# Kernel tuning notes

Hardware: AMD Instinct MI355X
Metric: run time of the kernel (lower is better)

Reference implementation:

```python
import jax, jax.numpy as jnp
import numpy as np

B, N, DIM, H, DH = 1, 2048, 1024, 16, 64


def setup_inputs() -> dict:
    key = jax.random.key(0)
    k1, k2, k3 = jax.random.split(key, 3)
    x = jax.random.normal(k1, (B, N, DIM), dtype=jnp.float32)
    # LinearNoBias(dim, 6*heads*dim_head): weight [6*H*DH, DIM]
    w_qkv = jax.random.normal(k2, (6 * H * DH, DIM), dtype=jnp.float32) * (DIM ** -0.5)
    # LinearNoBias(heads*dim_head, dim): weight [DIM, H*DH]
    w_out = jax.random.normal(k3, (DIM, H * DH), dtype=jnp.float32) * ((H * DH) ** -0.5)
    return {"x": x, "w_qkv": w_qkv, "w_out": w_out}


def reference(x, w_qkv, w_out):
    b, n, _ = x.shape
    scale = DH ** -0.5
    qkvs = x @ w_qkv.T  # [b, n, 6*H*DH]
    # rearrange 'b n (qkv h d) -> qkv b h n d'
    qkvs = qkvs.reshape(b, n, 6, H, DH).transpose(2, 0, 3, 1, 4)
    qu, ku, vu, qc, kc, vc = qkvs
    qu = qu * scale
    qc = qc * scale

    upper = jnp.triu(jnp.ones((n, n), dtype=bool), 1)  # strict upper triangle

    # term1: causal (lower-incl-diag) qc . vu
    term1 = jnp.einsum('bhid,bhjd->bhij', qc, vu)
    term1 = jnp.where(upper, 0.0, term1)

    # sigmoid lookahead term: strict-upper only
    sig = jax.nn.sigmoid(jnp.einsum('bhid,bhjd->bhij', qu, ku))
    sig = jnp.where(upper, sig, 0.0)

    Su = jnp.einsum('bhij,bhkj->bhik', term1, sig)

    Sc = jnp.einsum('bhid,bhjd->bhij', qc, kc)
    neg = -jnp.finfo(Sc.dtype).max
    Sc = jnp.where(upper, neg, Sc)

    scores = Sc - jax.nn.silu(Su)
    attn = jax.nn.softmax(scores, axis=-1)
    out = jnp.einsum('bhij,bhjd->bhid', attn, vc)  # [b,h,n,d]
    out = out.transpose(0, 2, 1, 3).reshape(b, n, H * DH)
    return out @ w_out.T
```

## Files before the change

### kernel.cpp

```cpp
#include <hip/hip_runtime.h>

using f16 = _Float16;
using half8  = __attribute__((ext_vector_type(8))) f16;
using half4v = __attribute__((ext_vector_type(4))) f16;
using float4v = __attribute__((ext_vector_type(4))) float;

#define DEV static __device__ __forceinline__

constexpr int N = 2048, DIM = 1024, H = 16, DH = 64, F6 = 6144;
constexpr int LDSH = 136;
constexpr int TS = 128 * 128;
constexpr int NTILES = 136;
constexpr int KD = 2048 * 64;


DEV int PL(int i, int k) { return i * (i + 1) / 2 + k; }
DEV int PU(int a, int b) { return a * 16 - a * (a - 1) / 2 + (b - a); }

template<int ROWS, int THREADS>
DEV void stage64(const f16* __restrict__ g, int strideHalves, f16* lds, int tid) {
#pragma unroll
  for (int q = 0; q < (ROWS * 8) / THREADS; ++q) {
    const int chunk = q * THREADS + tid;
    const int m = chunk >> 3, c = (chunk & 7) ^ (m & 7);
    const f16* gp = g + (size_t)m * strideHalves + c * 8;
    __builtin_amdgcn_global_load_lds(
        (const __attribute__((address_space(1))) unsigned int*)gp,
        (__attribute__((address_space(3))) unsigned int*)(lds + chunk * 8), 16, 0, 0);
  }
}

template<int ELEMS, int THREADS>
DEV void stage_panel(const f16* __restrict__ g, f16* lds, int tid) {
#pragma unroll
  for (int i = 0; i < ELEMS / 8 / THREADS; ++i) {
    const int chunk = i * THREADS + tid;
    __builtin_amdgcn_global_load_lds(
        (const __attribute__((address_space(1))) unsigned int*)(g + (size_t)chunk * 8),
        (__attribute__((address_space(3))) unsigned int*)(lds + chunk * 8), 16, 0, 0);
  }
}

DEV half8 rdfrag(const f16* T, int m, int ks, int q) {
  const int c = (ks * 4 + q) ^ (m & 7);
  return *(const half8*)(T + m * 64 + c * 8);
}

DEV void wfrag(f16* T, int row, int col, f16 v) {
  T[row * 64 + ((((col >> 3) ^ (row & 7)) << 3) | (col & 7))] = v;
}

DEV void gemm64(const f16* As, const f16* Bs, int wm, int wn, int l, float4v acc[4][4]) {
  const int q = l >> 4, mm = l & 15;
#pragma unroll
  for (int ks = 0; ks < 2; ++ks) {
    half8 af[4], bf[4];
#pragma unroll
    for (int mi = 0; mi < 4; ++mi) af[mi] = rdfrag(As, wm + mm + mi * 16, ks, q);
#pragma unroll
    for (int ni = 0; ni < 4; ++ni) bf[ni] = rdfrag(Bs, wn + mm + ni * 16, ks, q);
#pragma unroll
    for (int mi = 0; mi < 4; ++mi)
#pragma unroll
      for (int ni = 0; ni < 4; ++ni)
        acc[mi][ni] = __builtin_amdgcn_mfma_f32_16x16x32_f16(af[mi], bf[ni], acc[mi][ni], 0, 0, 0);
  }
}

DEV void decode_pair(int p, int& ti, int& tk) {
  int t = (int)((sqrtf(8.f * p + 1.f) - 1.f) * 0.5f);
  while (t * (t + 1) / 2 > p) --t;
  while ((t + 1) * (t + 2) / 2 <= p) ++t;
  const int i2 = p - t * (t + 1) / 2;
  ti = (15 - t) + i2;
  tk = i2;
}

__global__ __launch_bounds__(256) void k_cast(const float* __restrict__ s, f16* __restrict__ d, int n4) {
  int i = blockIdx.x * 256 + threadIdx.x;
  if (i < n4) {
    float4 v = ((const float4*)s)[i];
    half4v h;
    h[0] = (f16)v.x; h[1] = (f16)v.y; h[2] = (f16)v.z; h[3] = (f16)v.w;
    ((half4v*)d)[i] = h;
  }
}

__global__ __launch_bounds__(256) void k_qkv(const f16* __restrict__ xh, const f16* __restrict__ wh,
                                             f16* __restrict__ quh, f16* __restrict__ kuh,
                                             f16* __restrict__ vuh, f16* __restrict__ qch,
                                             f16* __restrict__ kch, f16* __restrict__ vcT,
                                             f16* __restrict__ vuT) {
  __shared__ __align__(16) f16 lds[128 * LDSH];
  f16* As = lds; f16* Bs = lds + 128 * 64;
  const int tid = threadIdx.x, w = tid >> 6, l = tid & 63;
  const int tm = blockIdx.x * 128, tf = blockIdx.y * 128;
  const int wm = (w >> 1) * 64, wn = (w & 1) * 64;
  float4v acc[4][4] = {};
  for (int k0 = 0; k0 < DIM; k0 += 64) {
    stage64<128, 256>(xh + (size_t)tm * DIM + k0, DIM, As, tid);
    stage64<128, 256>(wh + (size_t)tf * DIM + k0, DIM, Bs, tid);
    __syncthreads();
    gemm64(As, Bs, wm, wn, l, acc);
    __syncthreads();
  }
  const int rbase = (l >> 4) * 4, cidx = l & 15;
  const int t = tf >> 10;
  const float sc = (t == 0 || t == 3) ? 0.125f : 1.f;
  if (t == 5 || t == 2) {
#pragma unroll
    for (int mi = 0; mi < 4; ++mi)
#pragma unroll
      for (int ni = 0; ni < 4; ++ni) {
        const int f = tf + wn + ni * 16 + cidx;
        const int h = (f & 1023) >> 6, d = f & 63;
        const int n = tm + wm + mi * 16 + rbase;
        half4v p;
#pragma unroll
        for (int r = 0; r < 4; ++r) p[r] = (f16)acc[mi][ni][r];
        if (t == 5) {
          const int ks2 = (n & 63) >> 5, q2 = (n >> 3) & 3;
          const int inner = ks2 * 256 + q2 * 64 + (d >> 4) * 16 + (d & 15);
          *(half4v*)(vcT + (size_t)h * DH * N + (size_t)(n >> 6) * 4096 +
                     (size_t)inner * 8 + (n & 7)) = p;
        } else {
          *(half4v*)(vuT + ((size_t)h * DH + d) * N + n) = p;
        }
      }
  }
  if (t != 5) {
#pragma unroll
    for (int mi = 0; mi < 4; ++mi)
#pragma unroll
      for (int ni = 0; ni < 4; ++ni)
#pragma unroll
        for (int r = 0; r < 4; ++r)
          lds[(wm + mi * 16 + rbase + r) * LDSH + wn + ni * 16 + cidx] = (f16)(acc[mi][ni][r] * sc);
    __syncthreads();
    const int hb = (tf & 1023) >> 6;
    if (t == 4) {
#pragma unroll
      for (int qq = 0; qq < 8; ++qq) {
        const int idx = qq * 256 + tid;
        const int hh = idx >> 10, f = idx & 1023;
        const int pl = f >> 9, inner = f & 511;
        const int m2 = inner & 15, ni2 = (inner >> 4) & 3, q2 = (inner >> 6) & 3, ks2 = inner >> 8;
        const int row = pl * 64 + ni2 * 16 + m2;
        const int col = hh * 64 + ks2 * 32 + q2 * 8;
        *(half8*)(kch + (size_t)(hb + hh) * N * DH + ((size_t)(tm >> 6) + pl) * 4096 +
                  (size_t)inner * 8) = *(const half8*)(lds + row * LDSH + col);
      }
    } else {
      f16* dst = (t == 0) ? quh : (t == 1) ? kuh : (t == 2) ? vuh : qch;
#pragma unroll
      for (int q = 0; q < 8; ++q) {
        const int idx = q * 256 + tid, row = idx >> 4, c = idx & 15;
        const int h = hb + (c >> 3), d0 = (c & 7) * 8, n = tm + row;
        *(half8*)(dst + ((size_t)h * N + n) * DH + d0) = *(const half8*)(lds + row * LDSH + c * 8);
      }
    }
  }
}

__global__ __launch_bounds__(256) void k_dsig(const f16* __restrict__ quh, const f16* __restrict__ kuh,
                                              const f16* __restrict__ qch, const f16* __restrict__ vuh,
                                              const f16* __restrict__ vuT,
                                              f16* __restrict__ sigb, f16* __restrict__ DC,
                                              f16* __restrict__ diagb, int h0) {
  __shared__ __align__(16) f16 L[32768];
  f16* quA = L; f16* kuB = L + 8192; f16* s1 = L + 16384; f16* s2 = L + 24576;
  int b, a;
  decode_pair(blockIdx.y, b, a);
  const int hl = blockIdx.x, h = h0 + hl;
  const int tid = threadIdx.x, w = tid >> 6, l = tid & 63;
  const int q = l >> 4, m = l & 15;
  const int wm = (w >> 1) * 64, wn = (w & 1) * 64;
  const size_t ho = (size_t)h * N * DH;

  stage64<128, 256>(quh + ho + (size_t)(a * 128) * DH, DH, quA, tid);
  stage64<128, 256>(kuh + ho + (size_t)(b * 128) * DH, DH, kuB, tid);
  __syncthreads();
  float4v acc[4][4] = {};
  gemm64(quA, kuB, wm, wn, l, acc);
  __syncthreads();
  stage64<64, 256>(vuT + (size_t)h * DH * N + b * 128, N, kuB, tid);
  stage64<64, 256>(vuT + (size_t)h * DH * N + b * 128 + 64, N, kuB + 4096, tid);
#pragma unroll
  for (int mi = 0; mi < 4; ++mi)
#pragma unroll
    for (int ni = 0; ni < 4; ++ni)
#pragma unroll
      for (int r = 0; r < 4; ++r) {
        const int row = wm + mi * 16 + q * 4 + r;
        const int col = wn + ni * 16 + m;
        const float x = acc[mi][ni][r];
        const f16 sv = (b * 128 + col > a * 128 + row)
                           ? (f16)__builtin_amdgcn_rcpf(1.f + __expf(-x)) : (f16)0.f;
        wfrag((col < 64) ? s1 : s2, row, col & 63, sv);
      }
  __syncthreads();
  {
    f16* Sg = sigb + ((size_t)hl * NTILES + PU(a, b)) * TS;
#pragma unroll
    for (int qq = 0; qq < 8; ++qq) {
      const int idx = qq * 256 + tid;
      const int hf = idx >> 10, inner = idx & 1023;
      const int m2 = inner & 15, ni2 = (inner >> 4) & 3, q2 = (inner >> 6) & 3, ks2 = inner >> 8;
      const int row = hf * 64 + ni2 * 16 + m2;
      const int c8 = ks2 * 4 + q2;
      const f16* p = ((c8 >> 3) ? s2 : s1) + row * 64 + (((c8 & 7) ^ (row & 7)) << 3);
      *(half8*)(Sg + (size_t)idx * 8) = *(const half8*)p;
    }
  }
  float4v dacc[2][4] = {};
#pragma unroll
  for (int p = 0; p < 2; ++p)
#pragma unroll
    for (int ks = 0; ks < 2; ++ks) {
      half8 bf[4], af[2];
#pragma unroll
      for (int ni = 0; ni < 4; ++ni) bf[ni] = rdfrag(kuB + p * 4096, ni * 16 + m, ks, q);
#pragma unroll
      for (int mi = 0; mi < 2; ++mi) af[mi] = rdfrag(p ? s2 : s1, w * 32 + mi * 16 + m, ks, q);
#pragma unroll
      for (int mi = 0; mi < 2; ++mi)
#pragma unroll
        for (int ni = 0; ni < 4; ++ni)
          dacc[mi][ni] = __builtin_amdgcn_mfma_f32_16x16x32_f16(af[mi], bf[ni], dacc[mi][ni], 0, 0, 0);
    }
  __syncthreads();
  if (a == b) {
    stage64<128, 256>(qch + ho + (size_t)(a * 128) * DH, DH, quA, tid);
    stage64<128, 256>(vuh + ho + (size_t)(a * 128) * DH, DH, kuB, tid);
  }
  {
    f16* epsD = s1;
#pragma unroll
    for (int mi = 0; mi < 2; ++mi)
#pragma unroll
      for (int ni = 0; ni < 4; ++ni)
#pragma unroll
        for (int r = 0; r < 4; ++r)
          epsD[(w * 32 + mi * 16 + q * 4 + r) * 68 + ni * 16 + m] = (f16)dacc[mi][ni][r];
    __syncthreads();
    f16* Dg = DC + ((size_t)hl * 16 + b) * KD + (size_t)a * 8192;
#pragma unroll
    for (int qq = 0; qq < 4; ++qq) {
      const int idx = qq * 256 + tid;
      const int pl = idx >> 9, inner = idx & 511;
      const int m2 = inner & 15, ni2 = (inner >> 4) & 3, q2 = (inner >> 6) & 3, ks2 = inner >> 8;
      const int row = pl * 64 + ni2 * 16 + m2;
      const int c = ks2 * 4 + q2;
      *(half8*)(Dg + (size_t)idx * 8) = *(const half8*)(epsD + row * 68 + c * 8);
    }
  }
  if (a == b) {
    float4v tacc[4][4] = {};
    gemm64(quA, kuB, wm, wn, l, tacc);
    f16* Tg = diagb + ((size_t)hl * 16 + a) * TS;
#pragma unroll
    for (int mi = 0; mi < 4; ++mi)
#pragma unroll
      for (int ni = 0; ni < 4; ++ni)
#pragma unroll
        for (int r = 0; r < 4; ++r) {
          const int row = wm + mi * 16 + q * 4 + r, col = wn + ni * 16 + m;
          Tg[(size_t)row * 128 + col] = (col <= row) ? (f16)tacc[mi][ni][r] : (f16)0.f;
        }
  }
}

__global__ __launch_bounds__(256) void k_scan(f16* __restrict__ DC, int total) {
  const int idx = blockIdx.x * 256 + threadIdx.x;
  if (idx >= total) return;
  const int g = idx >> 17, off = idx & (KD - 1);
  const int a = off >> 13;
  f16* p = DC + (size_t)g * 16 * KD + off;
  float s = 0.f;
#pragma unroll
  for (int T = 0; T < 16; ++T) {
    const float v = (T >= a) ? (float)p[(size_t)T * KD] : 0.f;
    p[(size_t)T * KD] = (f16)s;
    s += v;
  }
}

__global__ __launch_bounds__(256) void k_favs(const f16* __restrict__ qch, const f16* __restrict__ kch,
                                              const f16* __restrict__ DC, const f16* __restrict__ sigb,
                                              const f16* __restrict__ diagb, const f16* __restrict__ vcT,
                                              f16* __restrict__ Oh, int h0) {
  __shared__ __align__(16) f16 L[2 * 16384 + 4 * 1024];
  const int hl = blockIdx.x, h = h0 + hl;
  const int y = (int)blockIdx.y;
  const int mt = (y < 32) ? (63 - y) : (y - 32);
  const int tid = threadIdx.x, w = tid >> 6, l = tid & 63;
  const int q = l >> 4, m = l & 15;
  const int d = w >> 1;
  const int rw = w & 1;
  const int ti = mt >> 2, r0 = mt * 32;
  const size_t ho = (size_t)h * N * DH;
  const f16* qc = qch + ho;
  const f16* kcb = kch + ho;
  const f16* Cb = DC + ((size_t)hl * 16 + ti) * KD;
  const f16* Td = diagb + ((size_t)hl * 16 + ti) * TS;
  const f16* Sgb = sigb + (size_t)hl * NTILES * TS;
  const f16* V = vcT + (size_t)h * DH * N;
  f16* pw = L + 32768 + w * 1024;
  const int lo = q * 512 + m * 8;
  constexpr float L2E = 1.44269504f;
  constexpr float THR2 = 11.5416f;

  const int rr = rw * 16 + m;
  half8 qcA[2], tdA[4];
  const int dr = (mt & 3) * 32 + rr;
#pragma unroll
  for (int ks = 0; ks < 2; ++ks)
    qcA[ks] = *(const half8*)(qc + (size_t)(r0 + rr) * DH + ks * 32 + q * 8);
#pragma unroll
  for (int ks = 0; ks < 4; ++ks)
    tdA[ks] = *(const half8*)(Td + (size_t)dr * 128 + ks * 32 + q * 8);

  float4v o[4] = {};
  float mrun[4], lrun[4];
#pragma unroll
  for (int r = 0; r < 4; ++r) { mrun[r] = -1e30f; lrun[r] = 0.f; }

  const int jtmax = mt >> 1;
  const int np = jtmax / 2 + 1;
  stage_panel<16384, 256>(Sgb + (size_t)PU(0, ti) * TS, L, tid);
  half8 cC[2][4];
  {
    int c0 = d; if (c0 > jtmax) c0 = 0;
    const f16* Cp = Cb + (size_t)c0 * 4096 + lo;
#pragma unroll
    for (int ks = 0; ks < 2; ++ks)
#pragma unroll
      for (int ni = 0; ni < 4; ++ni) cC[ks][ni] = *(const half8*)(Cp + ks * 2048 + ni * 128);
  }

  for (int p = 0; p < np; ++p) {
    const int pn = (p + 1 <= ti) ? (p + 1) : ti;
    stage_panel<16384, 256>(Sgb + (size_t)PU(pn, ti) * TS,
                            L + ((p + 1) & 1) * 16384, tid);
    half8 nC[2][4];
    {
      int c2 = 2 * (p + 1) + d; if (c2 > jtmax) c2 = 0;
      const f16* Cp = Cb + (size_t)c2 * 4096 + lo;
#pragma unroll
      for (int ks = 0; ks < 2; ++ks)
#pragma unroll
        for (int ni = 0; ni < 4; ++ni) nC[ks][ni] = *(const half8*)(Cp + ks * 2048 + ni * 128);
    }
    asm volatile("s_waitcnt vmcnt(16)" ::: "memory");
    __builtin_amdgcn_s_barrier();
    __builtin_amdgcn_sched_barrier(0);

    const int c = 2 * p + d;
    if (c <= jtmax) {
      const f16* Sp = L + (p & 1) * 16384 + d * 8192 + lo;
      const f16* Kp = kcb + (size_t)c * 4096 + lo;
      const f16* Vp = V + (size_t)c * 4096 + lo;
      half8 bK[2][4];
#pragma unroll
      for (int ks = 0; ks < 2; ++ks)
#pragma unroll
        for (int ni = 0; ni < 4; ++ni) bK[ks][ni] = *(const half8*)(Kp + ks * 2048 + ni * 128);
      float4v s[4] = {};
#pragma unroll
      for (int ks = 0; ks < 2; ++ks)
#pragma unroll
        for (int ni = 0; ni < 4; ++ni)
          s[ni] = __builtin_amdgcn_mfma_f32_16x16x32_f16(qcA[ks], cC[ks][ni], s[ni], 0, 0, 0);
#pragma unroll
      for (int ks = 0; ks < 4; ++ks) {
        half8 bf[4];
#pragma unroll
        for (int ni = 0; ni < 4; ++ni) bf[ni] = *(const half8*)(Sp + ks * 2048 + ni * 128);
#pragma unroll
        for (int ni = 0; ni < 4; ++ni)
          s[ni] = __builtin_amdgcn_mfma_f32_16x16x32_f16(tdA[ks], bf[ni], s[ni], 0, 0, 0);
      }
      half8 bV[2][4];
#pragma unroll
      for (int ks = 0; ks < 2; ++ks)
#pragma unroll
        for (int ni = 0; ni < 4; ++ni) bV[ks][ni] = *(const half8*)(Vp + ks * 2048 + ni * 128);
#pragma unroll
      for (int ni = 0; ni < 4; ++ni)
#pragma unroll
        for (int r = 0; r < 4; ++r) {
          const float x = s[ni][r];
          s[ni][r] = -x * __builtin_amdgcn_rcpf(1.f + __expf(-x));
        }
#pragma unroll
      for (int ks = 0; ks < 2; ++ks)
#pragma unroll
        for (int ni = 0; ni < 4; ++ni)
          s[ni] = __builtin_amdgcn_mfma_f32_16x16x32_f16(qcA[ks], bK[ks][ni], s[ni], 0, 0, 0);
      if (c == jtmax) {
        const int k0 = c * 64;
#pragma unroll
        for (int ni = 0; ni < 4; ++ni) {
          const int col = k0 + ni * 16 + m;
#pragma unroll
          for (int r = 0; r < 4; ++r) {
            const int gr = r0 + rw * 16 + q * 4 + r;
            if (col > gr) s[ni][r] = -1e30f;
          }
        }
      }
#pragma unroll
      for (int ni = 0; ni < 4; ++ni)
#pragma unroll
        for (int r = 0; r < 4; ++r) s[ni][r] *= L2E;
      float ts[4];
#pragma unroll
      for (int r = 0; r < 4; ++r) {
        float tmx = fmaxf(fmaxf(s[0][r], s[1][r]), fmaxf(s[2][r], s[3][r]));
#pragma unroll
        for (int x = 1; x < 16; x <<= 1) tmx = fmaxf(tmx, __shfl_xor(tmx, x));
        if (tmx > mrun[r] + THR2) {
          const float al = __builtin_amdgcn_exp2f(mrun[r] - tmx);
          mrun[r] = tmx;
          lrun[r] *= al;
#pragma unroll
          for (int ni = 0; ni < 4; ++ni) o[ni][r] *= al;
        }
        ts[r] = 0.f;
      }
#pragma unroll
      for (int ni = 0; ni < 4; ++ni)
#pragma unroll
        for (int r = 0; r < 4; ++r) {
          const float pp = __builtin_amdgcn_exp2f(s[ni][r] - mrun[r]);
          wfrag(pw, q * 4 + r, ni * 16 + m, (f16)pp);
          ts[r] += pp;
        }
#pragma unroll
      for (int r = 0; r < 4; ++r) {
#pragma unroll
        for (int x = 1; x < 16; x <<= 1) ts[r] += __shfl_xor(ts[r], x);
        lrun[r] += ts[r];
      }
#pragma unroll
      for (int ks = 0; ks < 2; ++ks) {
        half8 af = rdfrag(pw, m, ks, q);
#pragma unroll
        for (int ni = 0; ni < 4; ++ni)
          o[ni] = __builtin_amdgcn_mfma_f32_16x16x32_f16(af, bV[ks][ni], o[ni], 0, 0, 0);
      }
    }
    __builtin_amdgcn_sched_barrier(0);
    __builtin_amdgcn_s_barrier();
#pragma unroll
    for (int ks = 0; ks < 2; ++ks)
#pragma unroll
      for (int ni = 0; ni < 4; ++ni) cC[ks][ni] = nC[ks][ni];
  }

  asm volatile("s_waitcnt vmcnt(0)" ::: "memory");
  __builtin_amdgcn_s_barrier();

  float* OB = (float*)L;
  float* MB = (float*)L + 2 * 16 * 68;
  float* LB = MB + 2 * 16;
  if (d == 1) {
#pragma unroll
    for (int ni = 0; ni < 4; ++ni)
#pragma unroll
      for (int r = 0; r < 4; ++r)
        OB[(rw * 16 + q * 4 + r) * 68 + ni * 16 + m] = o[ni][r];
    if (m == 0)
#pragma unroll
      for (int r = 0; r < 4; ++r) {
        MB[rw * 16 + q * 4 + r] = mrun[r];
        LB[rw * 16 + q * 4 + r] = lrun[r];
      }
  }
  __syncthreads();
  if (d == 0) {
#pragma unroll
    for (int r = 0; r < 4; ++r) {
      const int row = q * 4 + r;
      const float m2 = MB[rw * 16 + row], l2 = LB[rw * 16 + row];
      const float ms = fmaxf(mrun[r], m2);
      const float e1 = __builtin_amdgcn_exp2f(mrun[r] - ms);
      const float e2 = __builtin_amdgcn_exp2f(m2 - ms);
      const float inv = __builtin_amdgcn_rcpf(lrun[r] * e1 + l2 * e2);
      const int gr = r0 + rw * 16 + row;
#pragma unroll
      for (int ni = 0; ni < 4; ++ni) {
        const float ov = o[ni][r] * e1 + OB[(rw * 16 + row) * 68 + ni * 16 + m] * e2;
        Oh[(size_t)gr * (H * DH) + h * DH + ni * 16 + m] = (f16)(ov * inv);
      }
    }
  }
}

__global__ __launch_bounds__(256) void k_out(const f16* __restrict__ Oh, const f16* __restrict__ wo,
                                             float* __restrict__ out) {
  __shared__ __align__(16) f16 lds[128 * LDSH];
  f16* As = lds; f16* Bs = lds + 128 * 64;
  const int tid = threadIdx.x, w = tid >> 6, l = tid & 63;
  const int tm = blockIdx.x * 128, tn = blockIdx.y * 128;
  const int wm = (w >> 1) * 64, wn = (w & 1) * 64;
  float4v acc[4][4] = {};
  for (int k0 = 0; k0 < DIM; k0 += 64) {
    stage64<128, 256>(Oh + (size_t)tm * DIM + k0, DIM, As, tid);
    stage64<128, 256>(wo + (size_t)tn * DIM + k0, DIM, Bs, tid);
    __syncthreads();
    gemm64(As, Bs, wm, wn, l, acc);
    __syncthreads();
  }
  const int rbase = (l >> 4) * 4, cidx = l & 15;
#pragma unroll
  for (int mi = 0; mi < 4; ++mi)
#pragma unroll
    for (int ni = 0; ni < 4; ++ni)
#pragma unroll
      for (int r = 0; r < 4; ++r) {
        const int n = tm + wm + mi * 16 + rbase + r;
        const int dmo = tn + wn + ni * 16 + cidx;
        out[(size_t)n * DIM + dmo] = acc[mi][ni][r];
      }
}

extern "C" void kernel_launch(void* const* d_in, const int* in_sizes, int n_in,
                              void* d_out, int out_size, void* d_ws, size_t ws_size,
                              hipStream_t stream) {
  const float* x = (const float*)d_in[0];
  const float* wqkv = (const float*)d_in[1];
  const float* wout = (const float*)d_in[2];
  float* out = (float*)d_out;
  char* ws = (char*)d_ws;

  size_t off = 0;
  auto alloc = [&](size_t b) { size_t o = off; off += (b + 255) & ~(size_t)255; return o; };
  f16* xh  = (f16*)(ws + alloc((size_t)N * DIM * 2));
  f16* wqh = (f16*)(ws + alloc((size_t)F6 * DIM * 2));
  f16* woh = (f16*)(ws + alloc((size_t)DIM * H * DH * 2));
  f16* quh = (f16*)(ws + alloc((size_t)H * N * DH * 2));
  f16* kuh = (f16*)(ws + alloc((size_t)H * N * DH * 2));
  f16* vuh = (f16*)(ws + alloc((size_t)H * N * DH * 2));
  f16* qch = (f16*)(ws + alloc((size_t)H * N * DH * 2));
  f16* kch = (f16*)(ws + alloc((size_t)H * N * DH * 2));
  f16* vcT = (f16*)(ws + alloc((size_t)H * DH * N * 2));
  f16* vuT = (f16*)(ws + alloc((size_t)H * DH * N * 2));
  f16* Oh  = (f16*)(ws + alloc((size_t)N * H * DH * 2));
  const size_t persist = off;

  const size_t per_head = ((size_t)NTILES * TS + (size_t)16 * KD + (size_t)16 * TS) * 2;
  int G = (ws_size > persist + 4096) ? (int)((ws_size - persist - 4096) / per_head) : 1;
  if (G < 1) G = 1;
  if (G > 16) G = 16;
  {
    const int R = (H + G - 1) / G;
    G = (H + R - 1) / R;
  }
  f16* sigb  = (f16*)(ws + alloc((size_t)G * NTILES * TS * 2));
  f16* DC    = (f16*)(ws + alloc((size_t)G * 16 * KD * 2));
  f16* diagb = (f16*)(ws + alloc((size_t)G * 16 * TS * 2));

  k_cast<<<(N * DIM / 4 + 255) / 256, 256, 0, stream>>>(x, xh, N * DIM / 4);
  k_cast<<<(F6 * DIM / 4 + 255) / 256, 256, 0, stream>>>(wqkv, wqh, F6 * DIM / 4);
  k_cast<<<(DIM * H * DH / 4 + 255) / 256, 256, 0, stream>>>(wout, woh, DIM * H * DH / 4);

  k_qkv<<<dim3(N / 128, F6 / 128), 256, 0, stream>>>(xh, wqh, quh, kuh, vuh, qch, kch, vcT, vuT);

  for (int h0 = 0; h0 < H; h0 += G) {
    const int Gr = (H - h0 < G) ? (H - h0) : G;
    k_dsig<<<dim3(Gr, 136), 256, 0, stream>>>(quh, kuh, qch, vuh, vuT, sigb, DC, diagb, h0);
    k_scan<<<(Gr * KD + 255) / 256, 256, 0, stream>>>(DC, Gr * KD);
    k_favs<<<dim3(Gr, 64), 256, 0, stream>>>(qch, kch, DC, sigb, diagb, vcT, Oh, h0);
  }

  k_out<<<dim3(16, 8), 256, 0, stream>>>(Oh, woh, out);
}
```

Measured before the change: 283.0 us.

## Split favs key range across two blocks per row tile and merge partials

Each row tile of the attention kernel is now handled by two blocks that each process half of the key panels. Each block writes unnormalized fp32 partial outputs plus running max and sum, and a new merge kernel combines them into fp16 Oh. This doubles the grid to improve occupancy and load balance on the causal triangle. The cost is extra global traffic for the partials, one more launch, and the lazy rescale threshold being replaced by an unconditional rescale.

New measurement: 280.9 us. No clear change (-0.7%).

```diff
diff --git a/kernel.cpp b/kernel.cpp
--- a/kernel.cpp
+++ b/kernel.cpp
@@ -288,11 +288,13 @@
 __global__ __launch_bounds__(256) void k_favs(const f16* __restrict__ qch, const f16* __restrict__ kch,
                                               const f16* __restrict__ DC, const f16* __restrict__ sigb,
                                               const f16* __restrict__ diagb, const f16* __restrict__ vcT,
-                                              f16* __restrict__ Oh, int h0) {
+                                              float* __restrict__ Opart, float* __restrict__ mpart,
+                                              float* __restrict__ lpart, int h0) {
   __shared__ __align__(16) f16 L[2 * 16384 + 4 * 1024];
   const int hl = blockIdx.x, h = h0 + hl;
   const int y = (int)blockIdx.y;
-  const int mt = (y < 32) ? (63 - y) : (y - 32);
+  const int mt = 63 - (y >> 1);
+  const int hf = y & 1;
   const int tid = threadIdx.x, w = tid >> 6, l = tid & 63;
   const int q = l >> 4, m = l & 15;
   const int d = w >> 1;
@@ -308,7 +310,6 @@
   f16* pw = L + 32768 + w * 1024;
   const int lo = q * 512 + m * 8;
   constexpr float L2E = 1.44269504f;
-  constexpr float THR2 = 11.5416f;
 
   const int rr = rw * 16 + m;
   half8 qcA[2], tdA[4];
@@ -327,10 +328,14 @@
 
   const int jtmax = mt >> 1;
   const int np = jtmax / 2 + 1;
-  stage_panel<16384, 256>(Sgb + (size_t)PU(0, ti) * TS, L, tid);
+  const int p0 = hf ? (np + 1) / 2 : 0;
+  const int p1 = hf ? np : (np + 1) / 2;
+
+  const int ps0 = (p0 <= ti) ? p0 : ti;
+  stage_panel<16384, 256>(Sgb + (size_t)PU(ps0, ti) * TS, L + (p0 & 1) * 16384, tid);
   half8 cC[2][4];
   {
-    int c0 = d; if (c0 > jtmax) c0 = 0;
+    int c0 = 2 * p0 + d; if (c0 > jtmax) c0 = 0;
     const f16* Cp = Cb + (size_t)c0 * 4096 + lo;
 #pragma unroll
     for (int ks = 0; ks < 2; ++ks)
@@ -338,7 +343,7 @@
       for (int ni = 0; ni < 4; ++ni) cC[ks][ni] = *(const half8*)(Cp + ks * 2048 + ni * 128);
   }
 
-  for (int p = 0; p < np; ++p) {
+  for (int p = p0; p < p1; ++p) {
     const int pn = (p + 1 <= ti) ? (p + 1) : ti;
     stage_panel<16384, 256>(Sgb + (size_t)PU(pn, ti) * TS,
                             L + ((p + 1) & 1) * 16384, tid);
@@ -419,13 +424,12 @@
         float tmx = fmaxf(fmaxf(s[0][r], s[1][r]), fmaxf(s[2][r], s[3][r]));
 #pragma unroll
         for (int x = 1; x < 16; x <<= 1) tmx = fmaxf(tmx, __shfl_xor(tmx, x));
-        if (tmx > mrun[r] + THR2) {
-          const float al = __builtin_amdgcn_exp2f(mrun[r] - tmx);
-          mrun[r] = tmx;
-          lrun[r] *= al;
-#pragma unroll
-          for (int ni = 0; ni < 4; ++ni) o[ni][r] *= al;
-        }
+        const float nm = fmaxf(mrun[r], tmx);
+        const float al = __builtin_amdgcn_exp2f(mrun[r] - nm);
+        mrun[r] = nm;
+        lrun[r] *= al;
+#pragma unroll
+        for (int ni = 0; ni < 4; ++ni) o[ni][r] *= al;
         ts[r] = 0.f;
       }
 #pragma unroll
@@ -479,6 +483,9 @@
   }
   __syncthreads();
   if (d == 0) {
+    float* Op = Opart + (size_t)(hl * 2 + hf) * N * 64;
+    float* Mp = mpart + (hl * 2 + hf) * N;
+    float* Lp = lpart + (hl * 2 + hf) * N;
 #pragma unroll
     for (int r = 0; r < 4; ++r) {
       const int row = q * 4 + r;
@@ -486,14 +493,41 @@
       const float ms = fmaxf(mrun[r], m2);
       const float e1 = __builtin_amdgcn_exp2f(mrun[r] - ms);
       const float e2 = __builtin_amdgcn_exp2f(m2 - ms);
-      const float inv = __builtin_amdgcn_rcpf(lrun[r] * e1 + l2 * e2);
       const int gr = r0 + rw * 16 + row;
-#pragma unroll
-      for (int ni = 0; ni < 4; ++ni) {
-        const float ov = o[ni][r] * e1 + OB[(rw * 16 + row) * 68 + ni * 16 + m] * e2;
-        Oh[(size_t)gr * (H * DH) + h * DH + ni * 16 + m] = (f16)(ov * inv);
-      }
+      if (m == 0) { Mp[gr] = ms; Lp[gr] = lrun[r] * e1 + l2 * e2; }
+#pragma unroll
+      for (int ni = 0; ni < 4; ++ni)
+        Op[(size_t)gr * 64 + ni * 16 + m] =
+            o[ni][r] * e1 + OB[(rw * 16 + row) * 68 + ni * 16 + m] * e2;
     }
+  }
+}
+
+__global__ __launch_bounds__(256) void k_merge(const float* __restrict__ Opart,
+                                               const float* __restrict__ mpart,
+                                               const float* __restrict__ lpart,
+                                               f16* __restrict__ Oh, int h0) {
+  const int hl = blockIdx.x, h = h0 + hl;
+  const float* O0 = Opart + (size_t)(hl * 2 + 0) * N * 64;
+  const float* O1 = Opart + (size_t)(hl * 2 + 1) * N * 64;
+#pragma unroll
+  for (int it = 0; it < 2; ++it) {
+    const int idx = (int)blockIdx.y * 512 + it * 256 + threadIdx.x;
+    const int row = idx >> 4, c4 = idx & 15;
+    const float m0 = mpart[(hl * 2 + 0) * N + row], m1 = mpart[(hl * 2 + 1) * N + row];
+    const float l0 = lpart[(hl * 2 + 0) * N + row], l1 = lpart[(hl * 2 + 1) * N + row];
+    const float ms = fmaxf(m0, m1);
+    const float e0 = __builtin_amdgcn_exp2f(m0 - ms);
+    const float e1 = __builtin_amdgcn_exp2f(m1 - ms);
+    const float inv = __builtin_amdgcn_rcpf(l0 * e0 + l1 * e1);
+    const float4 a = ((const float4*)(O0 + (size_t)row * 64))[c4];
+    const float4 b = ((const float4*)(O1 + (size_t)row * 64))[c4];
+    half4v o4;
+    o4[0] = (f16)((a.x * e0 + b.x * e1) * inv);
+    o4[1] = (f16)((a.y * e0 + b.y * e1) * inv);
+    o4[2] = (f16)((a.z * e0 + b.z * e1) * inv);
+    o4[3] = (f16)((a.w * e0 + b.w * e1) * inv);
+    *(half4v*)(Oh + (size_t)row * (H * DH) + h * DH + c4 * 4) = o4;
   }
 }
 
@@ -549,7 +583,8 @@
   f16* Oh  = (f16*)(ws + alloc((size_t)N * H * DH * 2));
   const size_t persist = off;
 
-  const size_t per_head = ((size_t)NTILES * TS + (size_t)16 * KD + (size_t)16 * TS) * 2;
+  const size_t per_head = ((size_t)NTILES * TS + (size_t)16 * KD + (size_t)16 * TS) * 2 +
+                          (size_t)2 * N * 64 * 4 + (size_t)4 * N * 4;
   int G = (ws_size > persist + 4096) ? (int)((ws_size - persist - 4096) / per_head) : 1;
   if (G < 1) G = 1;
   if (G > 16) G = 16;
@@ -560,6 +595,9 @@
   f16* sigb  = (f16*)(ws + alloc((size_t)G * NTILES * TS * 2));
   f16* DC    = (f16*)(ws + alloc((size_t)G * 16 * KD * 2));
   f16* diagb = (f16*)(ws + alloc((size_t)G * 16 * TS * 2));
+  float* Opart = (float*)(ws + alloc((size_t)G * 2 * N * 64 * 4));
+  float* mpart = (float*)(ws + alloc((size_t)G * 2 * N * 4));
+  float* lpart = (float*)(ws + alloc((size_t)G * 2 * N * 4));
 
   k_cast<<<(N * DIM / 4 + 255) / 256, 256, 0, stream>>>(x, xh, N * DIM / 4);
   k_cast<<<(F6 * DIM / 4 + 255) / 256, 256, 0, stream>>>(wqkv, wqh, F6 * DIM / 4);
@@ -571,7 +609,9 @@
     const int Gr = (H - h0 < G) ? (H - h0) : G;
     k_dsig<<<dim3(Gr, 136), 256, 0, stream>>>(quh, kuh, qch, vuh, vuT, sigb, DC, diagb, h0);
     k_scan<<<(Gr * KD + 255) / 256, 256, 0, stream>>>(DC, Gr * KD);
-    k_favs<<<dim3(Gr, 64), 256, 0, stream>>>(qch, kch, DC, sigb, diagb, vcT, Oh, h0);
+    k_favs<<<dim3(Gr, 128), 256, 0, stream>>>(qch, kch, DC, sigb, diagb, vcT,
+                                              Opart, mpart, lpart, h0);
+    k_merge<<<dim3(Gr, 64), 256, 0, stream>>>(Opart, mpart, lpart, Oh, h0);
   }
 
   k_out<<<dim3(16, 8), 256, 0, stream>>>(Oh, woh, out);
```

## Compute softmax row sums via MFMA with ones vector; simplify rescale and tile order

Applied to the files above, without the earlier changes.

Replaces the shuffle-based per-row sum of probabilities with an extra MFMA against a ones vector, so the denominator accumulates in a matrix accumulator alongside the output. It also drops the lazy-rescale threshold in favour of always rescaling to the running max, and changes block-to-tile ordering to plain descending work order. This removes cross-lane reductions per tile at the cost of one extra MFMA per k-step and unconditional exp/rescale work. The row sum now comes from f16-rounded probabilities, which may slightly change accuracy.

Result: faster. 263.5 us (-6.9%).

```diff
diff --git a/kernel.cpp b/kernel.cpp
--- a/kernel.cpp
+++ b/kernel.cpp
@@ -291,8 +291,7 @@
                                               f16* __restrict__ Oh, int h0) {
   __shared__ __align__(16) f16 L[2 * 16384 + 4 * 1024];
   const int hl = blockIdx.x, h = h0 + hl;
-  const int y = (int)blockIdx.y;
-  const int mt = (y < 32) ? (63 - y) : (y - 32);
+  const int mt = 63 - (int)blockIdx.y;
   const int tid = threadIdx.x, w = tid >> 6, l = tid & 63;
   const int q = l >> 4, m = l & 15;
   const int d = w >> 1;
@@ -308,7 +307,6 @@
   f16* pw = L + 32768 + w * 1024;
   const int lo = q * 512 + m * 8;
   constexpr float L2E = 1.44269504f;
-  constexpr float THR2 = 11.5416f;
 
   const int rr = rw * 16 + m;
   half8 qcA[2], tdA[4];
@@ -320,10 +318,15 @@
   for (int ks = 0; ks < 4; ++ks)
     tdA[ks] = *(const half8*)(Td + (size_t)dr * 128 + ks * 32 + q * 8);
 
+  half8 ones;
+#pragma unroll
+  for (int e = 0; e < 8; ++e) ones[e] = (f16)1.f;
+
   float4v o[4] = {};
-  float mrun[4], lrun[4];
-#pragma unroll
-  for (int r = 0; r < 4; ++r) { mrun[r] = -1e30f; lrun[r] = 0.f; }
+  float4v o5 = {};
+  float mrun[4];
+#pragma unroll
+  for (int r = 0; r < 4; ++r) mrun[r] = -1e30f;
 
   const int jtmax = mt >> 1;
   const int np = jtmax / 2 + 1;
@@ -413,20 +416,17 @@
       for (int ni = 0; ni < 4; ++ni)
 #pragma unroll
         for (int r = 0; r < 4; ++r) s[ni][r] *= L2E;
-      float ts[4];
 #pragma unroll
       for (int r = 0; r < 4; ++r) {
         float tmx = fmaxf(fmaxf(s[0][r], s[1][r]), fmaxf(s[2][r], s[3][r]));
 #pragma unroll
         for (int x = 1; x < 16; x <<= 1) tmx = fmaxf(tmx, __shfl_xor(tmx, x));
-        if (tmx > mrun[r] + THR2) {
-          const float al = __builtin_amdgcn_exp2f(mrun[r] - tmx);
-          mrun[r] = tmx;
-          lrun[r] *= al;
-#pragma unroll
-          for (int ni = 0; ni < 4; ++ni) o[ni][r] *= al;
-        }
-        ts[r] = 0.f;
+        const float nm = fmaxf(mrun[r], tmx);
+        const float al = __builtin_amdgcn_exp2f(mrun[r] - nm);
+        mrun[r] = nm;
+        o5[r] *= al;
+#pragma unroll
+        for (int ni = 0; ni < 4; ++ni) o[ni][r] *= al;
       }
 #pragma unroll
       for (int ni = 0; ni < 4; ++ni)
@@ -434,20 +434,14 @@
         for (int r = 0; r < 4; ++r) {
           const float pp = __builtin_amdgcn_exp2f(s[ni][r] - mrun[r]);
           wfrag(pw, q * 4 + r, ni * 16 + m, (f16)pp);
-          ts[r] += pp;
         }
-#pragma unroll
-      for (int r = 0; r < 4; ++r) {
-#pragma unroll
-        for (int x = 1; x < 16; x <<= 1) ts[r] += __shfl_xor(ts[r], x);
-        lrun[r] += ts[r];
-      }
 #pragma unroll
       for (int ks = 0; ks < 2; ++ks) {
         half8 af = rdfrag(pw, m, ks, q);
 #pragma unroll
         for (int ni = 0; ni < 4; ++ni)
           o[ni] = __builtin_amdgcn_mfma_f32_16x16x32_f16(af, bV[ks][ni], o[ni], 0, 0, 0);
+        o5 = __builtin_amdgcn_mfma_f32_16x16x32_f16(af, ones, o5, 0, 0, 0);
       }
     }
     __builtin_amdgcn_sched_barrier(0);
@@ -474,7 +468,7 @@
 #pragma unroll
       for (int r = 0; r < 4; ++r) {
         MB[rw * 16 + q * 4 + r] = mrun[r];
-        LB[rw * 16 + q * 4 + r] = lrun[r];
+        LB[rw * 16 + q * 4 + r] = o5[r];
       }
   }
   __syncthreads();
@@ -486,7 +480,7 @@
       const float ms = fmaxf(mrun[r], m2);
       const float e1 = __builtin_amdgcn_exp2f(mrun[r] - ms);
       const float e2 = __builtin_amdgcn_exp2f(m2 - ms);
-      const float inv = __builtin_amdgcn_rcpf(lrun[r] * e1 + l2 * e2);
+      const float inv = __builtin_amdgcn_rcpf(o5[r] * e1 + l2 * e2);
       const int gr = r0 + rw * 16 + row;
 #pragma unroll
       for (int ni = 0; ni < 4; ++ni) {
```
